# Kernel optimization log

Hardware: AMD Instinct MI355X
Metric: run time of the kernel (lower is better)

## Reference

```python
import jax, jax.numpy as jnp
import numpy as np

IN_FEATURES = 4096
OUT_FEATURES = 4096
GROUP_SIZE = 128


def _unpack_int4_last_dim(packed):
    # packed: [..., P] int32 -> [..., P*8] int32 nibbles in [0,15]
    shifts = jnp.arange(0, 32, 4, dtype=jnp.int32)
    u = (packed[..., None] >> shifts) & 15
    return u.reshape(*packed.shape[:-1], packed.shape[-1] * 8)


def setup_inputs() -> dict:
    key = jax.random.key(0)
    k1, k2, k3, k4, k5 = jax.random.split(key, 5)
    groups = IN_FEATURES // GROUP_SIZE  # 32
    x = jax.random.normal(k1, (4096, IN_FEATURES), dtype=jnp.float32)
    qweight = jax.random.randint(k2, (OUT_FEATURES, IN_FEATURES // 8), 0, 2147483647, dtype=jnp.int32)
    qzeros = jax.random.randint(k3, (OUT_FEATURES, groups // 8), 0, 2147483647, dtype=jnp.int32)
    scales = jax.random.uniform(k4, (OUT_FEATURES, groups), dtype=jnp.float32) * 0.02 + 0.001
    bias = jax.random.normal(k5, (OUT_FEATURES,), dtype=jnp.float32)
    return {"x": x, "qweight": qweight, "qzeros": qzeros, "scales": scales, "bias": bias}


def _dequantize_weight(qweight, qzeros, scales):
    # qweight: [out, in/8] -> w_int: [out, in]
    w_int = _unpack_int4_last_dim(qweight).astype(jnp.float32)
    # qzeros: [out, groups/8] -> zeros: [out, groups]
    zeros = _unpack_int4_last_dim(qzeros).astype(jnp.float32)
    group_ids = jnp.arange(IN_FEATURES) // GROUP_SIZE  # [in]
    # expand per-group scale/zero along in_features
    w = (w_int - zeros[:, group_ids]) * scales[:, group_ids]  # [out, in]
    return w


def reference(x, qweight, qzeros, scales, bias):
    w = _dequantize_weight(qweight, qzeros, scales)  # [out, in] fp32
    return x @ w.T + bias  # [tokens, out]
```

## Files before the change

### kernel.cpp

```cpp
#include <hip/hip_runtime.h>
#include <hip/hip_bf16.h>

#define TOKENS 4096
#define IN_F   4096
#define OUT_F  4096

typedef __bf16 bf16x8 __attribute__((ext_vector_type(8)));
typedef float  f32x4  __attribute__((ext_vector_type(4)));
typedef unsigned int u32;
typedef u32 u32x4 __attribute__((ext_vector_type(4)));

#define DEQ_BLOCKS 2048
#define CVT_BLOCKS 4096

__device__ __forceinline__ void gld_lds16(const void* g, void* l) {
    __builtin_amdgcn_global_load_lds(
        (const __attribute__((address_space(1))) u32*)g,
        (__attribute__((address_space(3))) u32*)l,
        16, 0, 0);
}

__global__ __launch_bounds__(256) void prep_kernel(
        const u32* __restrict__ qweight, const u32* __restrict__ qzeros,
        const float* __restrict__ scales, const float* __restrict__ x,
        __bf16* __restrict__ W, __bf16* __restrict__ A) {
    const int tid = threadIdx.x;
    if (blockIdx.x < DEQ_BLOCKS) {
        int idx4 = blockIdx.x * 256 + tid;
        int n  = idx4 >> 7;
        int p4 = (idx4 & 127) << 2;
        int g  = p4 >> 4;
        u32 qz = qzeros[(n << 2) + (g >> 3)];
        float z = (float)((qz >> ((g & 7) * 4)) & 15);
        float s = scales[(n << 5) + g];
        u32x4 qw = *(const u32x4*)(qweight + (size_t)n * 512 + p4);
        __bf16* dst = W + (size_t)n * IN_F + p4 * 8;
#pragma unroll
        for (int c = 0; c < 4; ++c) {
            bf16x8 h;
#pragma unroll
            for (int j = 0; j < 8; ++j) {
                float w = ((float)((qw[c] >> (4 * j)) & 15) - z) * s;
                h[j] = (__bf16)w;
            }
            *(bf16x8*)(dst + c * 8) = h;
        }
    } else {
        int idx = (blockIdx.x - DEQ_BLOCKS) * 256 + tid;
        const f32x4* xp = (const f32x4*)x + (size_t)idx * 4;
        f32x4 v0 = xp[0], v1 = xp[1], v2 = xp[2], v3 = xp[3];
        bf16x8 h0, h1;
#pragma unroll
        for (int j = 0; j < 4; ++j) {
            h0[j] = (__bf16)v0[j]; h0[4 + j] = (__bf16)v1[j];
            h1[j] = (__bf16)v2[j]; h1[4 + j] = (__bf16)v3[j];
        }
        bf16x8* ap = (bf16x8*)A + (size_t)idx * 2;
        ap[0] = h0; ap[1] = h1;
    }
}

__global__ __launch_bounds__(512, 2) void gemm8p(
        const __bf16* __restrict__ A, const __bf16* __restrict__ B,
        const float* __restrict__ bias, float* __restrict__ C) {
    __shared__ __align__(16) char lsA[65536];
    __shared__ __align__(16) char lsB[65536];

    const int t    = threadIdx.x;
    const int lane = t & 63, wave = t >> 6;
    const int lr   = lane & 15, quad = lane >> 4;
    const int wm   = (wave >> 2) * 128;
    const int wn   = (wave & 3) * 64;

    int bid = blockIdx.x;
    bid = (bid & 7) * 32 + (bid >> 3);
    const int bm = bid >> 4, bn = bid & 15;

    const __bf16* Abase = A + (size_t)bm * 256 * IN_F;
    const __bf16* Bbase = B + (size_t)bn * 256 * IN_F;

    const int srow0 = t >> 2;
    const int srow1 = 128 + (t >> 2);
    const int scol0 = ((t & 3) ^ ((srow0 >> 1) & 3)) * 8;
    const int scol1 = ((t & 3) ^ ((srow1 >> 1) & 3)) * 8;

#define STAGE(OPBASE, LS, KT, KH, BUF) do {                                  \
    int _kb = (((KT) & 63) * 64 + (KH) * 32);                                \
    gld_lds16(OPBASE + (size_t)srow0 * IN_F + _kb + scol0,                   \
              LS + ((BUF) * 2 + (KH)) * 16384 + t * 16);                     \
    gld_lds16(OPBASE + (size_t)srow1 * IN_F + _kb + scol1,                   \
              LS + ((BUF) * 2 + (KH)) * 16384 + 8192 + t * 16);              \
} while (0)

    const u32 slot16 = (u32)((quad ^ ((lr >> 1) & 3)) * 16);
    const u32 lsA0 = (u32)(size_t)(__attribute__((address_space(3))) char*)lsA;
    const u32 lsB0 = (u32)(size_t)(__attribute__((address_space(3))) char*)lsB;
    const u32 aA = lsA0 + (u32)((wm + lr) * 64) + slot16;
    const u32 aB = lsB0 + (u32)((wn + lr) * 64) + slot16;

    bf16x8 af[4], bfr[4];
    f32x4 acc[8][4] = {};

#define DSR(dst, base, OFF) do {                                             \
    u32x4 _r;                                                                \
    asm volatile("ds_read_b128 %0, %1 offset:%2"                             \
                 : "=v"(_r) : "v"(base), "n"(OFF));                          \
    dst = __builtin_bit_cast(bf16x8, _r);                                    \
} while (0)

#define LDA4(PM, KH, BUF) do {                                               \
    DSR(af[0], aA, (((BUF)*2+(KH))*16384 + (PM)*4096 + 0*1024));             \
    DSR(af[1], aA, (((BUF)*2+(KH))*16384 + (PM)*4096 + 1*1024));             \
    DSR(af[2], aA, (((BUF)*2+(KH))*16384 + (PM)*4096 + 2*1024));             \
    DSR(af[3], aA, (((BUF)*2+(KH))*16384 + (PM)*4096 + 3*1024));             \
} while (0)

#define LDB4(KH, BUF) do {                                                   \
    DSR(bfr[0], aB, (((BUF)*2+(KH))*16384 + 0*1024));                        \
    DSR(bfr[1], aB, (((BUF)*2+(KH))*16384 + 1*1024));                        \
    DSR(bfr[2], aB, (((BUF)*2+(KH))*16384 + 2*1024));                        \
    DSR(bfr[3], aB, (((BUF)*2+(KH))*16384 + 3*1024));                        \
} while (0)

#define MFMA16(PM) do {                                                      \
    _Pragma("unroll")                                                        \
    for (int i = 0; i < 4; ++i)                                              \
    _Pragma("unroll")                                                        \
    for (int j = 0; j < 4; ++j)                                              \
        acc[(PM) * 4 + i][j] = __builtin_amdgcn_mfma_f32_16x16x32_bf16(      \
            af[i], bfr[j], acc[(PM) * 4 + i][j], 0, 0, 0);                   \
} while (0)

#define FENCE() asm volatile("" ::: "memory")
#define BAR()  do { FENCE(); __builtin_amdgcn_s_barrier(); FENCE(); } while (0)
#define VM4()  asm volatile("s_waitcnt vmcnt(4)" ::: "memory")
#define PRIO(x) __builtin_amdgcn_s_setprio(x)
#define OPENB() do { BAR();                                                  \
    asm volatile("s_waitcnt lgkmcnt(0)" ::: "memory");                       \
    __builtin_amdgcn_sched_barrier(0); } while (0)

    STAGE(Abase, lsA, 0, 0, 0);
    STAGE(Bbase, lsB, 0, 0, 0);
    STAGE(Abase, lsA, 0, 1, 0);
    STAGE(Bbase, lsB, 0, 1, 0);
    STAGE(Abase, lsA, 1, 0, 1);
    STAGE(Bbase, lsB, 1, 0, 1);
    VM4();
    BAR();

#define TILE(KT, B) do {                                                     \
                          \
    LDB4(0, B); LDA4(0, 0, B);                                               \
    STAGE(Abase, lsA, (KT) + 1, 1, 1 - (B));                                 \
    OPENB(); PRIO(1); MFMA16(0); PRIO(0); BAR();                             \
                        \
    LDA4(1, 0, B);                                                           \
    STAGE(Bbase, lsB, (KT) + 1, 1, 1 - (B));                                 \
    OPENB(); PRIO(1); MFMA16(1); PRIO(0); BAR();                             \
        \
    LDB4(1, B); LDA4(0, 1, B);                                               \
    STAGE(Abase, lsA, (KT) + 2, 0, B);                                       \
    OPENB(); PRIO(1); MFMA16(0); PRIO(0); BAR();                             \
              \
    LDA4(1, 1, B);                                                           \
    STAGE(Bbase, lsB, (KT) + 2, 0, B);                                       \
    OPENB(); PRIO(1); MFMA16(1); PRIO(0); VM4(); BAR();                      \
} while (0)

    for (int kt = 0; kt < 64; kt += 2) {
        TILE(kt, 0);
        TILE(kt + 1, 1);
    }

    asm volatile("s_waitcnt vmcnt(0)" ::: "memory");

    const int row0 = bm * 256 + wm + quad * 4;
    const int col0 = bn * 256 + wn + lr;
#pragma unroll
    for (int j = 0; j < 4; ++j) {
        const int col = col0 + j * 16;
        const float bv = bias[col];
#pragma unroll
        for (int i = 0; i < 8; ++i) {
            const int row = row0 + i * 16;
#pragma unroll
            for (int r = 0; r < 4; ++r)
                C[(size_t)(row + r) * OUT_F + col] = acc[i][j][r] + bv;
        }
    }
}

extern "C" void kernel_launch(void* const* d_in, const int* in_sizes, int n_in,
                              void* d_out, int out_size, void* d_ws, size_t ws_size,
                              hipStream_t stream) {
    (void)in_sizes; (void)n_in; (void)out_size; (void)ws_size;
    const float* x       = (const float*)d_in[0];
    const u32*   qweight = (const u32*)d_in[1];
    const u32*   qzeros  = (const u32*)d_in[2];
    const float* scales  = (const float*)d_in[3];
    const float* bias    = (const float*)d_in[4];
    float* out = (float*)d_out;

    __bf16* W   = (__bf16*)d_ws;
    __bf16* Abf = (__bf16*)((char*)d_ws + (size_t)OUT_F * IN_F * 2);

    prep_kernel<<<dim3(DEQ_BLOCKS + CVT_BLOCKS), dim3(256), 0, stream>>>(
        qweight, qzeros, scales, x, W, Abf);
    gemm8p<<<dim3(256), dim3(512), 0, stream>>>(Abf, W, bias, out);
}
```

Measured before the change: 247.5 us.

## Interleave LDS fragment reads with MFMAs and prefetch next phase operands

Restructures the GEMM main loop so that each phase issues the LDS reads for the next phase's A/B fragments between groups of MFMAs, instead of reading all fragments up front and then doing a barrier-plus-lgkmcnt wait before the MFMA block. This software-pipelines ds_read latency behind matrix math and removes one barrier per phase. The wait counts are adjusted (vmcnt 6/4) to match the new ordering. It relies on careful register reuse, since fragment registers are overwritten right after their last MFMA use, and it moves the point where other waves' LDS writes must be visible.

```diff
diff --git a/kernel.cpp b/kernel.cpp
--- a/kernel.cpp
+++ b/kernel.cpp
@@ -101,6 +101,9 @@
     bf16x8 af[4], bfr[4];
     f32x4 acc[8][4] = {};
 
+#define RA(BUF, KH) (((BUF) * 2 + (KH)) * 16384)
+#define RB(BUF, KH) (((BUF) * 2 + (KH)) * 16384)
+
 #define DSR(dst, base, OFF) do {                                             \
     u32x4 _r;                                                                \
     asm volatile("ds_read_b128 %0, %1 offset:%2"                             \
@@ -108,36 +111,72 @@
     dst = __builtin_bit_cast(bf16x8, _r);                                    \
 } while (0)
 
-#define LDA4(PM, KH, BUF) do {                                               \
-    DSR(af[0], aA, (((BUF)*2+(KH))*16384 + (PM)*4096 + 0*1024));             \
-    DSR(af[1], aA, (((BUF)*2+(KH))*16384 + (PM)*4096 + 1*1024));             \
-    DSR(af[2], aA, (((BUF)*2+(KH))*16384 + (PM)*4096 + 2*1024));             \
-    DSR(af[3], aA, (((BUF)*2+(KH))*16384 + (PM)*4096 + 3*1024));             \
-} while (0)
-
-#define LDB4(KH, BUF) do {                                                   \
-    DSR(bfr[0], aB, (((BUF)*2+(KH))*16384 + 0*1024));                        \
-    DSR(bfr[1], aB, (((BUF)*2+(KH))*16384 + 1*1024));                        \
-    DSR(bfr[2], aB, (((BUF)*2+(KH))*16384 + 2*1024));                        \
-    DSR(bfr[3], aB, (((BUF)*2+(KH))*16384 + 3*1024));                        \
-} while (0)
-
-#define MFMA16(PM) do {                                                      \
+#define MFMA4_I(PM, I) do {                                                  \
+    _Pragma("unroll")                                                        \
+    for (int j = 0; j < 4; ++j)                                              \
+        acc[(PM) * 4 + (I)][j] = __builtin_amdgcn_mfma_f32_16x16x32_bf16(    \
+            af[(I)], bfr[j], acc[(PM) * 4 + (I)][j], 0, 0, 0);               \
+} while (0)
+
+#define MFMA4_J(PM, J) do {                                                  \
     _Pragma("unroll")                                                        \
     for (int i = 0; i < 4; ++i)                                              \
-    _Pragma("unroll")                                                        \
-    for (int j = 0; j < 4; ++j)                                              \
-        acc[(PM) * 4 + i][j] = __builtin_amdgcn_mfma_f32_16x16x32_bf16(      \
-            af[i], bfr[j], acc[(PM) * 4 + i][j], 0, 0, 0);                   \
+        acc[(PM) * 4 + i][(J)] = __builtin_amdgcn_mfma_f32_16x16x32_bf16(    \
+            af[i], bfr[(J)], acc[(PM) * 4 + i][(J)], 0, 0, 0);               \
 } while (0)
 
 #define FENCE() asm volatile("" ::: "memory")
 #define BAR()  do { FENCE(); __builtin_amdgcn_s_barrier(); FENCE(); } while (0)
+#define VM6()  asm volatile("s_waitcnt vmcnt(6)" ::: "memory")
 #define VM4()  asm volatile("s_waitcnt vmcnt(4)" ::: "memory")
 #define PRIO(x) __builtin_amdgcn_s_setprio(x)
-#define OPENB() do { BAR();                                                  \
-    asm volatile("s_waitcnt lgkmcnt(0)" ::: "memory");                       \
-    __builtin_amdgcn_sched_barrier(0); } while (0)
+#define SB()   __builtin_amdgcn_sched_barrier(0)
+#define LGKM0SB() do {                                                       \
+    asm volatile("s_waitcnt lgkmcnt(0)" ::: "memory"); SB(); } while (0)
+
+#define P0_BODY(KT, B) do {                                                  \
+    STAGE(Abase, lsA, (KT) + 1, 1, 1 - (B));                                 \
+    LGKM0SB(); PRIO(1);                                                      \
+    MFMA4_I(0,0); SB(); DSR(af[0], aA, RA(B,0)+4096+0*1024); SB();           \
+    MFMA4_I(0,1); SB(); DSR(af[1], aA, RA(B,0)+4096+1*1024); SB();           \
+    MFMA4_I(0,2); SB(); DSR(af[2], aA, RA(B,0)+4096+2*1024); SB();           \
+    MFMA4_I(0,3); SB(); DSR(af[3], aA, RA(B,0)+4096+3*1024); SB();           \
+    PRIO(0); BAR();                                                          \
+} while (0)
+
+#define P1_BODY(KT, B) do {                                                  \
+    STAGE(Bbase, lsB, (KT) + 1, 1, 1 - (B));                                 \
+    LGKM0SB(); PRIO(1);                                                      \
+    MFMA4_J(1,0); SB(); DSR(bfr[0], aB, RB(B,1)+0*1024); SB();               \
+    MFMA4_J(1,1); SB(); DSR(bfr[1], aB, RB(B,1)+1*1024); SB();               \
+    MFMA4_J(1,2); SB(); DSR(bfr[2], aB, RB(B,1)+2*1024); SB();               \
+    MFMA4_J(1,3); SB(); DSR(bfr[3], aB, RB(B,1)+3*1024); SB();               \
+    DSR(af[0], aA, RA(B,1)+0*1024); DSR(af[1], aA, RA(B,1)+1*1024);          \
+    DSR(af[2], aA, RA(B,1)+2*1024); DSR(af[3], aA, RA(B,1)+3*1024);          \
+    PRIO(0); BAR();                                                          \
+} while (0)
+
+#define P2_BODY(KT, B) do {                                                  \
+    STAGE(Abase, lsA, (KT) + 2, 0, (B));                                     \
+    LGKM0SB(); PRIO(1);                                                      \
+    MFMA4_I(0,0); SB(); DSR(af[0], aA, RA(B,1)+4096+0*1024); SB();           \
+    MFMA4_I(0,1); SB(); DSR(af[1], aA, RA(B,1)+4096+1*1024); SB();           \
+    MFMA4_I(0,2); SB(); DSR(af[2], aA, RA(B,1)+4096+2*1024); SB();           \
+    MFMA4_I(0,3); SB(); DSR(af[3], aA, RA(B,1)+4096+3*1024); SB();           \
+    PRIO(0); VM6(); BAR();                                                   \
+} while (0)
+
+#define P3_BODY(KT, B) do {                                                  \
+    STAGE(Bbase, lsB, (KT) + 2, 0, (B));                                     \
+    LGKM0SB(); PRIO(1);                                                      \
+    MFMA4_J(1,0); SB(); DSR(bfr[0], aB, RB(1-(B),0)+0*1024); SB();           \
+    MFMA4_J(1,1); SB(); DSR(bfr[1], aB, RB(1-(B),0)+1*1024); SB();           \
+    MFMA4_J(1,2); SB(); DSR(bfr[2], aB, RB(1-(B),0)+2*1024); SB();           \
+    MFMA4_J(1,3); SB(); DSR(bfr[3], aB, RB(1-(B),0)+3*1024); SB();           \
+    DSR(af[0], aA, RA(1-(B),0)+0*1024); DSR(af[1], aA, RA(1-(B),0)+1*1024);  \
+    DSR(af[2], aA, RA(1-(B),0)+2*1024); DSR(af[3], aA, RA(1-(B),0)+3*1024);  \
+    PRIO(0); VM4(); BAR();                                                   \
+} while (0)
 
     STAGE(Abase, lsA, 0, 0, 0);
     STAGE(Bbase, lsB, 0, 0, 0);
@@ -147,32 +186,18 @@
     STAGE(Bbase, lsB, 1, 0, 1);
     VM4();
     BAR();
-
-#define TILE(KT, B) do {                                                     \
-                          \
-    LDB4(0, B); LDA4(0, 0, B);                                               \
-    STAGE(Abase, lsA, (KT) + 1, 1, 1 - (B));                                 \
-    OPENB(); PRIO(1); MFMA16(0); PRIO(0); BAR();                             \
-                        \
-    LDA4(1, 0, B);                                                           \
-    STAGE(Bbase, lsB, (KT) + 1, 1, 1 - (B));                                 \
-    OPENB(); PRIO(1); MFMA16(1); PRIO(0); BAR();                             \
-        \
-    LDB4(1, B); LDA4(0, 1, B);                                               \
-    STAGE(Abase, lsA, (KT) + 2, 0, B);                                       \
-    OPENB(); PRIO(1); MFMA16(0); PRIO(0); BAR();                             \
-              \
-    LDA4(1, 1, B);                                                           \
-    STAGE(Bbase, lsB, (KT) + 2, 0, B);                                       \
-    OPENB(); PRIO(1); MFMA16(1); PRIO(0); VM4(); BAR();                      \
-} while (0)
+    DSR(bfr[0], aB, RB(0,0)+0*1024); DSR(bfr[1], aB, RB(0,0)+1*1024);
+    DSR(bfr[2], aB, RB(0,0)+2*1024); DSR(bfr[3], aB, RB(0,0)+3*1024);
+    DSR(af[0], aA, RA(0,0)+0*1024);  DSR(af[1], aA, RA(0,0)+1*1024);
+    DSR(af[2], aA, RA(0,0)+2*1024);  DSR(af[3], aA, RA(0,0)+3*1024);
 
     for (int kt = 0; kt < 64; kt += 2) {
-        TILE(kt, 0);
-        TILE(kt + 1, 1);
+        P0_BODY(kt, 0); P1_BODY(kt, 0); P2_BODY(kt, 0); P3_BODY(kt, 0);
+        P0_BODY(kt + 1, 1); P1_BODY(kt + 1, 1);
+        P2_BODY(kt + 1, 1); P3_BODY(kt + 1, 1);
     }
 
-    asm volatile("s_waitcnt vmcnt(0)" ::: "memory");
+    asm volatile("s_waitcnt vmcnt(0) lgkmcnt(0)" ::: "memory");
 
     const int row0 = bm * 256 + wm + quad * 4;
     const int col0 = bn * 256 + wn + lr;
```

Measured after the change: 240.2 us. 1.03x faster.
